# Performance work log

Measured on AMD Instinct MI355X. Metric: run time of the kernel, lower is better.

## Reference

```python
import jax, jax.numpy as jnp
import numpy as np

B, H, W = 8, 64, 64
DIM1, DIM2 = 384, 256
NH, DH = 8, 32
INNER = NH * DH
EPS = 1e-5


def _layernorm(x, w, b):
    mu = jnp.mean(x, axis=-1, keepdims=True)
    var = jnp.mean((x - mu) ** 2, axis=-1, keepdims=True)
    return (x - mu) * jax.lax.rsqrt(var + EPS) * w + b


def _axial_attn(q, k, v, scale):
    # q,k,v: [B,H,W,nh,dh]; row attention over H, col attention over W
    sh = jnp.einsum('biwnd,bjwnd->bwnij', q, k) * scale  # [B,W,nh,H,H]
    oh = jnp.einsum('bwnij,bjwnd->biwnd', jax.nn.softmax(sh, axis=-1), v)
    sw = jnp.einsum('bhind,bhjnd->bhnij', q, k) * scale  # [B,H,nh,W,W]
    ow = jnp.einsum('bhnij,bhjnd->bhind', jax.nn.softmax(sw, axis=-1), v)
    return oh + ow  # [B,H,W,nh,dh]


def setup_inputs() -> dict:
    key = jax.random.key(0)
    ks = jax.random.split(key, 16)
    s1 = 1.0 / np.sqrt(DIM1)
    s2 = 1.0 / np.sqrt(DIM2)
    si = 1.0 / np.sqrt(INNER)
    return {
        'x1': jax.random.normal(ks[0], (B, DIM1, H, W), jnp.float32),
        'x2': jax.random.normal(ks[1], (B, DIM2, H, W), jnp.float32),
        'ln1q_w': jnp.ones((DIM1,), jnp.float32),
        'ln1q_b': jnp.zeros((DIM1,), jnp.float32),
        'ln2kv_w': jnp.ones((DIM2,), jnp.float32),
        'ln2kv_b': jnp.zeros((DIM2,), jnp.float32),
        'Wq1': jax.random.normal(ks[2], (DIM1, INNER), jnp.float32) * s1,
        'Wkv2': jax.random.normal(ks[3], (DIM2, 2 * INNER), jnp.float32) * s2,
        'Wout1': jax.random.normal(ks[4], (INNER, DIM2), jnp.float32) * si,
        'bout1': jnp.zeros((DIM2,), jnp.float32),
        'ln2q_w': jnp.ones((DIM2,), jnp.float32),
        'ln2q_b': jnp.zeros((DIM2,), jnp.float32),
        'ln1kv_w': jnp.ones((DIM1,), jnp.float32),
        'ln1kv_b': jnp.zeros((DIM1,), jnp.float32),
        'Wq2': jax.random.normal(ks[5], (DIM2, INNER), jnp.float32) * s2,
        'Wkv1': jax.random.normal(ks[6], (DIM1, 2 * INNER), jnp.float32) * s1,
        'Wout2': jax.random.normal(ks[7], (INNER, DIM2), jnp.float32) * si,
        'bout2': jnp.zeros((DIM2,), jnp.float32),
        'Wsc': jax.random.normal(ks[8], (DIM2, DIM1), jnp.float32) * s1,  # 1x1 conv [out,in]
        'bn_gamma': jnp.ones((DIM2,), jnp.float32),
        'bn_beta': jnp.zeros((DIM2,), jnp.float32),
        'bn_mean': jnp.zeros((DIM2,), jnp.float32),
        'bn_var': jnp.ones((DIM2,), jnp.float32),
    }


def reference(x1, x2, ln1q_w, ln1q_b, ln2kv_w, ln2kv_b, Wq1, Wkv2, Wout1, bout1,
              ln2q_w, ln2q_b, ln1kv_w, ln1kv_b, Wq2, Wkv1, Wout2, bout2,
              Wsc, bn_gamma, bn_beta, bn_mean, bn_var):
    b, c1, h, w = x1.shape
    scale = DH ** -0.5
    x1f = jnp.transpose(x1, (0, 2, 3, 1))  # [B,H,W,C1]
    x2f = jnp.transpose(x2, (0, 2, 3, 1))  # [B,H,W,C2]

    def heads(t):
        return t.reshape(b, h, w, NH, DH)

    # branch 1: q from x1, kv from x2
    q1 = _layernorm(x1f, ln1q_w, ln1q_b) @ Wq1
    kv2 = _layernorm(x2f, ln2kv_w, ln2kv_b) @ Wkv2
    k2, v2 = jnp.split(kv2, 2, axis=-1)
    o1 = _axial_attn(heads(q1), heads(k2), heads(v2), scale)
    fused1 = o1.reshape(b, h, w, INNER) @ Wout1 + bout1
    # shortcut: 1x1 conv + BN (inference stats)
    sc = jnp.einsum('bhwc,oc->bhwo', x1f, Wsc)
    sc = (sc - bn_mean) * jax.lax.rsqrt(bn_var + EPS) * bn_gamma + bn_beta
    y1 = sc + fused1

    # branch 2: q from x2, kv from x1
    q2 = _layernorm(x2f, ln2q_w, ln2q_b) @ Wq2
    kv1 = _layernorm(x1f, ln1kv_w, ln1kv_b) @ Wkv1
    k1, v1 = jnp.split(kv1, 2, axis=-1)
    o2 = _axial_attn(heads(q2), heads(k1), heads(v1), scale)
    fused2 = o2.reshape(b, h, w, INNER) @ Wout2 + bout2
    y2 = x2f + fused2

    out = y1 + y2  # [B,H,W,C2]
    return jnp.transpose(out, (0, 3, 1, 2))
```

## Files before the change

### kernel.cpp

```cpp
#include <hip/hip_runtime.h>

typedef unsigned short u16;
typedef unsigned int u32;
typedef float v4f __attribute__((ext_vector_type(4)));
typedef __bf16 v8bf __attribute__((ext_vector_type(8)));

__device__ __forceinline__ float bf2f(u16 v) {
  union { u32 u; float f; } x; x.u = ((u32)v) << 16; return x.f;
}
__device__ __forceinline__ u16 f2bf(float f) {
  union { float f; u32 u; } x; x.f = f;
  u32 u = x.u;
  return (u16)((u + 0x7FFFu + ((u >> 16) & 1u)) >> 16);
}
__device__ __forceinline__ u32 f2u(float f) {
  union { float f; u32 u; } x; x.f = f; return x.u;
}
__device__ __forceinline__ u32 pk2bf(float a, float b) {
  const u32 au = f2u(a) + 0x8000u;
  const u32 bu = f2u(b) + 0x8000u;
  return (bu & 0xFFFF0000u) | (au >> 16);
}

struct Ptrs { const void* p[23]; };

__global__ __launch_bounds__(256) void convert_all(Ptrs ps, u16* __restrict__ cx1,
                                                   u16* __restrict__ cx2,
                                                   u16* __restrict__ cw) {
  static const int sz[23]  = {12582912, 8388608, 384, 384, 256, 256, 98304, 131072,
                              65536, 256, 256, 256, 384, 384, 65536, 196608, 65536,
                              256, 98304, 256, 256, 256, 256};
  static const int off[23] = {0, 0, 0, 384, 768, 1024, 1280, 99584, 230656, 296192,
                              296448, 296704, 296960, 297344, 297728, 363264, 559872,
                              625408, 625664, 723968, 724224, 724480, 724736};
  const int ti = blockIdx.y;
  const int n8 = sz[ti] >> 3;
  const bool isf32 = (((const u32*)ps.p[2])[0] == 0x3F800000u);
  u16* dst = (ti == 0) ? cx1 : (ti == 1) ? cx2 : (cw + off[ti]);
  const void* src = ps.p[ti];
  const int stride = gridDim.x * blockDim.x;
  for (int i = blockIdx.x * blockDim.x + threadIdx.x; i < n8; i += stride) {
    if (isf32) {
      const float4 f0 = ((const float4*)src)[2*i];
      const float4 f1 = ((const float4*)src)[2*i + 1];
      u16 tmp[8];
      tmp[0] = f2bf(f0.x); tmp[1] = f2bf(f0.y); tmp[2] = f2bf(f0.z); tmp[3] = f2bf(f0.w);
      tmp[4] = f2bf(f1.x); tmp[5] = f2bf(f1.y); tmp[6] = f2bf(f1.z); tmp[7] = f2bf(f1.w);
      ((uint4*)dst)[i] = *(const uint4*)tmp;
    } else {
      ((uint4*)dst)[i] = ((const uint4*)src)[i];
    }
  }
}

__global__ void prep_bt(const u16* __restrict__ lnq_w, const u16* __restrict__ lnq_b,
                        const u16* __restrict__ lnkv_w, const u16* __restrict__ lnkv_b,
                        const u16* __restrict__ Wq, const u16* __restrict__ Wkv,
                        u16* __restrict__ BT, float* __restrict__ bias) {
  const int C = blockDim.x;
  const int j = blockIdx.x;
  const int c = threadIdx.x;
  float w, bco, wv;
  if (j < 256) { w = bf2f(lnq_w[c]); bco = bf2f(lnq_b[c]); wv = bf2f(Wq[c*256 + j]); }
  else         { w = bf2f(lnkv_w[c]); bco = bf2f(lnkv_b[c]); wv = bf2f(Wkv[c*512 + (j-256)]); }
  BT[(size_t)j*C + c] = f2bf(w * wv);
  __shared__ float red[384];
  red[c] = bco * wv;
  __syncthreads();
  if (c == 0) { float s = 0.f; for (int i = 0; i < C; i++) s += red[i]; bias[j] = s; }
}

__global__ void prep_fin(const u16* __restrict__ Wout1, const u16* __restrict__ Wout2,
                         const u16* __restrict__ Wsc, const u16* __restrict__ bout1,
                         const u16* __restrict__ bout2, const u16* __restrict__ gam,
                         const u16* __restrict__ bet, const u16* __restrict__ mean,
                         const u16* __restrict__ var, u16* __restrict__ BT,
                         float* __restrict__ bias) {
  const int o = blockIdx.x, t = threadIdx.x;
  const float g = rsqrtf(bf2f(var[o]) + 1e-5f) * bf2f(gam[o]);
  for (int idx = t; idx < 1408; idx += 256) {
    float v;
    if (idx < 512)       v = bf2f(Wout1[(idx & 255)*256 + o]);
    else if (idx < 1024) v = bf2f(Wout2[((idx - 512) & 255)*256 + o]);
    else                 v = bf2f(Wsc[o*384 + (idx - 1024)]) * g;
    BT[(size_t)o*1408 + idx] = f2bf(v);
  }
  if (t == 0) bias[o] = bf2f(bet[o]) - bf2f(mean[o])*g + bf2f(bout1[o]) + bf2f(bout2[o]);
}

__global__ __launch_bounds__(256) void ln_c384(const u16* __restrict__ x,
                                               u16* __restrict__ xn, u16* __restrict__ xraw) {
  __shared__ u16 tile[384*66];
  __shared__ float rsum[4][64], rsq[4][64], smean[64], srstd[64];
  const int t = threadIdx.x, w = t & 63, g = t >> 6;
  const int bh = blockIdx.x, b = bh >> 6, h = bh & 63;
  const u16* src = x + (size_t)b*384*4096 + h*64 + w;
  float sum = 0.f, sq = 0.f;
  for (int j = 0; j < 96; j++) {
    const int c = g*96 + j;
    const u16 uv = src[(size_t)c*4096];
    tile[c*66 + w] = uv;
    const float v = bf2f(uv); sum += v; sq += v*v;
  }
  rsum[g][w] = sum; rsq[g][w] = sq;
  __syncthreads();
  if (t < 64) {
    const float s = rsum[0][t]+rsum[1][t]+rsum[2][t]+rsum[3][t];
    const float q = rsq[0][t]+rsq[1][t]+rsq[2][t]+rsq[3][t];
    const float mean = s * (1.0f/384.0f);
    float var = q * (1.0f/384.0f) - mean*mean;
    if (var < 0.f) var = 0.f;
    smean[t] = mean; srstd[t] = rsqrtf(var + 1e-5f);
  }
  __syncthreads();
  const size_t pos0 = (size_t)bh * 64;
  for (int i = 0; i < 96; i++) {
    const int flat = i*256 + t;
    const int ww = flat / 384, c = flat - ww*384;
    const u16 uv = tile[c*66 + ww];
    const float v = (bf2f(uv) - smean[ww]) * srstd[ww];
    const size_t p = pos0 + ww;
    xn[p*384 + c] = f2bf(v);
    xraw[p*384 + c] = uv;
  }
}

__global__ __launch_bounds__(256) void ln_c256(const u16* __restrict__ x,
                                               u16* __restrict__ xn) {
  __shared__ u16 tile[256*66];
  __shared__ float rsum[4][64], rsq[4][64], smean[64], srstd[64];
  const int t = threadIdx.x, w = t & 63, g = t >> 6;
  const int bh = blockIdx.x, b = bh >> 6, h = bh & 63;
  const u16* src = x + (size_t)b*256*4096 + h*64 + w;
  float sum = 0.f, sq = 0.f;
  for (int j = 0; j < 64; j++) {
    const int c = g*64 + j;
    const u16 uv = src[(size_t)c*4096];
    tile[c*66 + w] = uv;
    const float v = bf2f(uv); sum += v; sq += v*v;
  }
  rsum[g][w] = sum; rsq[g][w] = sq;
  __syncthreads();
  if (t < 64) {
    const float s = rsum[0][t]+rsum[1][t]+rsum[2][t]+rsum[3][t];
    const float q = rsq[0][t]+rsq[1][t]+rsq[2][t]+rsq[3][t];
    const float mean = s * (1.0f/256.0f);
    float var = q * (1.0f/256.0f) - mean*mean;
    if (var < 0.f) var = 0.f;
    smean[t] = mean; srstd[t] = rsqrtf(var + 1e-5f);
  }
  __syncthreads();
  const size_t pos0 = (size_t)bh * 64;
  for (int i = 0; i < 64; i++) {
    const int flat = i*256 + t;
    const int ww = flat >> 8, c = flat & 255;
    const float v = (bf2f(tile[c*66 + ww]) - smean[ww]) * srstd[ww];
    xn[(pos0 + ww)*256 + c] = f2bf(v);
  }
}

__global__ __launch_bounds__(256) void gemm_bt(const u16* __restrict__ A,
                                               const u16* __restrict__ BT,
                                               u16* __restrict__ C,
                                               const float* __restrict__ bias,
                                               int N, int K) {
  __shared__ u16 lsA[128*40];
  __shared__ u16 lsB[128*40];
  const int t = threadIdx.x;
  const int m0 = blockIdx.x * 128, n0 = blockIdx.y * 128;
  const int lane = t & 63, wv = t >> 6;
  const int wm = wv & 1, wn = wv >> 1;
  const int lo = lane & 15, hi = lane >> 4;
  const int r0 = t >> 2, c8 = (t & 3) << 3;
  const u16* Ab = A + (size_t)(m0 + r0) * K + c8;
  const u16* Bb = BT + (size_t)(n0 + r0) * K + c8;
  v4f acc[4][4] = {};
  for (int kb = 0; kb < K; kb += 32) {
    uint4 a0 = *(const uint4*)(Ab + kb);
    uint4 a1 = *(const uint4*)(Ab + (size_t)64*K + kb);
    uint4 b0 = *(const uint4*)(Bb + kb);
    uint4 b1 = *(const uint4*)(Bb + (size_t)64*K + kb);
    __syncthreads();
    *(uint4*)&lsA[r0*40 + c8] = a0;
    *(uint4*)&lsA[(r0+64)*40 + c8] = a1;
    *(uint4*)&lsB[r0*40 + c8] = b0;
    *(uint4*)&lsB[(r0+64)*40 + c8] = b1;
    __syncthreads();
    v8bf av[4], bv[4];
#pragma unroll
    for (int i = 0; i < 4; i++) av[i] = *(const v8bf*)&lsA[(wm*64 + i*16 + lo)*40 + hi*8];
#pragma unroll
    for (int i = 0; i < 4; i++) bv[i] = *(const v8bf*)&lsB[(wn*64 + i*16 + lo)*40 + hi*8];
#pragma unroll
    for (int mt = 0; mt < 4; mt++)
#pragma unroll
      for (int nt = 0; nt < 4; nt++)
        acc[mt][nt] = __builtin_amdgcn_mfma_f32_16x16x32_bf16(av[mt], bv[nt], acc[mt][nt], 0, 0, 0);
  }
#pragma unroll
  for (int mt = 0; mt < 4; mt++) {
    const int row = m0 + wm*64 + mt*16 + hi*4;
#pragma unroll
    for (int nt = 0; nt < 4; nt++) {
      const int col = n0 + wn*64 + nt*16 + lo;
      const float bs = bias[col];
#pragma unroll
      for (int r = 0; r < 4; r++)
        C[(size_t)(row + r) * N + col] = f2bf(acc[mt][nt][r] + bs);
    }
  }
}

__global__ __launch_bounds__(256) void gemm_final(const u16* __restrict__ Ao,
                                                  const u16* __restrict__ Ar,
                                                  const u16* __restrict__ BT,
                                                  const float* __restrict__ bias,
                                                  const u16* __restrict__ x2c,
                                                  const u32* __restrict__ probe,
                                                  void* __restrict__ outv) {
  __shared__ u16 smem[16640];
  u16* lsA = smem;
  u16* lsB = smem + 5120;
  const int t = threadIdx.x;
  const int m0 = blockIdx.x * 128, n0 = blockIdx.y * 128;
  const int lane = t & 63, wv = t >> 6;
  const int wm = wv & 1, wn = wv >> 1;
  const int lo = lane & 15, hi = lane >> 4;
  const int r0 = t >> 2, c8 = (t & 3) << 3;
  const u16* AoR = Ao + (size_t)(m0 + r0) * 1024 + c8;
  const u16* ArR = Ar + (size_t)(m0 + r0) * 384 + c8;
  const u16* Bb  = BT + (size_t)(n0 + r0) * 1408 + c8;
  v4f acc[4][4] = {};
  for (int kb = 0; kb < 1408; kb += 32) {
    uint4 a0, a1;
    if (kb < 1024) { a0 = *(const uint4*)(AoR + kb); a1 = *(const uint4*)(AoR + 64*1024 + kb); }
    else { a0 = *(const uint4*)(ArR + (kb-1024)); a1 = *(const uint4*)(ArR + 64*384 + (kb-1024)); }
    uint4 b0 = *(const uint4*)(Bb + kb);
    uint4 b1 = *(const uint4*)(Bb + 64*1408 + kb);
    __syncthreads();
    *(uint4*)&lsA[r0*40 + c8] = a0;
    *(uint4*)&lsA[(r0+64)*40 + c8] = a1;
    *(uint4*)&lsB[r0*40 + c8] = b0;
    *(uint4*)&lsB[(r0+64)*40 + c8] = b1;
    __syncthreads();
    v8bf av[4], bv[4];
#pragma unroll
    for (int i = 0; i < 4; i++) av[i] = *(const v8bf*)&lsA[(wm*64 + i*16 + lo)*40 + hi*8];
#pragma unroll
    for (int i = 0; i < 4; i++) bv[i] = *(const v8bf*)&lsB[(wn*64 + i*16 + lo)*40 + hi*8];
#pragma unroll
    for (int mt = 0; mt < 4; mt++)
#pragma unroll
      for (int nt = 0; nt < 4; nt++)
        acc[mt][nt] = __builtin_amdgcn_mfma_f32_16x16x32_bf16(av[mt], bv[nt], acc[mt][nt], 0, 0, 0);
  }
  __syncthreads();
#pragma unroll
  for (int mt = 0; mt < 4; mt++)
#pragma unroll
    for (int nt = 0; nt < 4; nt++) {
      const int nl = wn*64 + nt*16 + lo;
      const float bs = bias[n0 + nl];
#pragma unroll
      for (int r = 0; r < 4; r++)
        smem[(wm*64 + mt*16 + hi*4 + r)*130 + nl] = f2bf(acc[mt][nt][r] + bs);
    }
  __syncthreads();
  const bool isf32 = (probe[0] == 0x3F800000u);
  const int bh0 = blockIdx.x * 2;
  for (int i = 0; i < 64; i++) {
    const int flat = i*256 + t;
    const int nl = flat >> 7;
    const int rem = flat & 127;
    const int mb = rem >> 6, w = rem & 63;
    const int bh = bh0 + mb, b = bh >> 6, h = bh & 63;
    const size_t oidx = ((size_t)(b*256 + n0 + nl)*64 + h)*64 + w;
    const float val = bf2f(smem[(mb*64 + w)*130 + nl]) + bf2f(x2c[oidx]);
    if (isf32) ((float*)outv)[oidx] = val;
    else       ((u16*)outv)[oidx]   = f2bf(val);
  }
}

__global__ __launch_bounds__(64) void attn(const u16* __restrict__ qkv1,
                                           const u16* __restrict__ qkv2,
                                           u16* __restrict__ Ao) {
  __shared__ u16 smem[7424];
  constexpr int LVT = 0, LQ = 2304, LK = 4864, LP = 2304, LO = 2304;
  const int t = threadIdx.x;
  const int lo = t & 15, quad = t >> 4;
  const int bx = blockIdx.x;
  const int head = blockIdx.y;
  const int z = blockIdx.z;
  const int br = z >> 1, dir = z & 1;
  const int b = bx >> 6, x = bx & 63;
  const u16* Qb  = (br == 0) ? qkv1 : qkv2;
  const u16* KVb = (br == 0) ? qkv2 : qkv1;
  const int qc = head*32, kc = 256 + head*32, vc = 512 + head*32;
  const int pbase = (dir == 0) ? (b*4096 + x) : ((b*64 + x)*64);
  const int pstr  = (dir == 0) ? 64 : 1;
  {
    const size_t p = (size_t)(pbase + t*pstr) * 768;
    const u16* qr = Qb + p + qc;
    const u16* kr = KVb + p + kc;
    const u16* vr = KVb + p + vc;
#pragma unroll
    for (int i = 0; i < 4; i++) *(uint4*)&smem[LQ + t*40 + i*8] = *(const uint4*)(qr + i*8);
#pragma unroll
    for (int i = 0; i < 4; i++) *(uint4*)&smem[LK + t*40 + i*8] = *(const uint4*)(kr + i*8);
    u16 vbuf[32];
#pragma unroll
    for (int i = 0; i < 4; i++) *(uint4*)&vbuf[i*8] = *(const uint4*)(vr + i*8);
#pragma unroll
    for (int d = 0; d < 32; d++) smem[LVT + d*72 + t] = vbuf[d];
  }
  __syncthreads();
  v4f s[4][4];
  {
    v8bf qa[4], ka[4];
#pragma unroll
    for (int i = 0; i < 4; i++) qa[i] = *(const v8bf*)&smem[LQ + (i*16 + lo)*40 + quad*8];
#pragma unroll
    for (int i = 0; i < 4; i++) ka[i] = *(const v8bf*)&smem[LK + (i*16 + lo)*40 + quad*8];
#pragma unroll
    for (int qt = 0; qt < 4; qt++)
#pragma unroll
      for (int kt = 0; kt < 4; kt++) {
        v4f z4 = {};
        s[qt][kt] = __builtin_amdgcn_mfma_f32_16x16x32_bf16(ka[kt], qa[qt], z4, 0, 0, 0);
      }
  }
  __syncthreads();
  const float scale = 0.17677669529663687f;
#pragma unroll
  for (int qt = 0; qt < 4; qt++) {
    float tv[16];
    float mx = -1e30f;
#pragma unroll
    for (int kt = 0; kt < 4; kt++)
#pragma unroll
      for (int r = 0; r < 4; r++) {
        const float v = s[qt][kt][r] * scale;
        tv[kt*4 + r] = v;
        mx = fmaxf(mx, v);
      }
    mx = fmaxf(mx, __shfl_xor(mx, 16));
    mx = fmaxf(mx, __shfl_xor(mx, 32));
    float sm = 0.f;
#pragma unroll
    for (int i = 0; i < 16; i++) { tv[i] = __expf(tv[i] - mx); sm += tv[i]; }
    sm += __shfl_xor(sm, 16);
    sm += __shfl_xor(sm, 32);
    const float inv = 1.0f / sm;
    const int q = qt*16 + lo;
#pragma unroll
    for (int kt = 0; kt < 4; kt++)
#pragma unroll
      for (int rp = 0; rp < 2; rp++) {
        const u32 pk = pk2bf(tv[kt*4 + rp*2] * inv, tv[kt*4 + rp*2 + 1] * inv);
        *(u32*)&smem[LP + q*72 + kt*16 + quad*4 + rp*2] = pk;
      }
  }
  __syncthreads();
  v4f o[2][4] = {};
  {
    v8bf va[2][2], pb[4][2];
#pragma unroll
    for (int mt = 0; mt < 2; mt++)
#pragma unroll
      for (int ks = 0; ks < 2; ks++)
        va[mt][ks] = *(const v8bf*)&smem[LVT + (mt*16 + lo)*72 + ks*32 + quad*8];
#pragma unroll
    for (int nt = 0; nt < 4; nt++)
#pragma unroll
      for (int ks = 0; ks < 2; ks++)
        pb[nt][ks] = *(const v8bf*)&smem[LP + (nt*16 + lo)*72 + ks*32 + quad*8];
#pragma unroll
    for (int mt = 0; mt < 2; mt++)
#pragma unroll
      for (int nt = 0; nt < 4; nt++) {
        o[mt][nt] = __builtin_amdgcn_mfma_f32_16x16x32_bf16(va[mt][0], pb[nt][0], o[mt][nt], 0, 0, 0);
        o[mt][nt] = __builtin_amdgcn_mfma_f32_16x16x32_bf16(va[mt][1], pb[nt][1], o[mt][nt], 0, 0, 0);
      }
  }
  __syncthreads();
#pragma unroll
  for (int mt = 0; mt < 2; mt++)
#pragma unroll
    for (int nt = 0; nt < 4; nt++)
#pragma unroll
      for (int rp = 0; rp < 2; rp++) {
        const u32 pk = pk2bf(o[mt][nt][rp*2], o[mt][nt][rp*2 + 1]);
        *(u32*)&smem[LO + (nt*16 + lo)*40 + mt*16 + quad*4 + rp*2] = pk;
      }
  __syncthreads();
  {
    const int oc = z*256 + head*32;
    const size_t gbase = (size_t)(pbase + t*pstr) * 1024 + oc;
#pragma unroll
    for (int i = 0; i < 4; i++)
      *(uint4*)&Ao[gbase + i*8] = *(const uint4*)&smem[LO + t*40 + i*8];
  }
}

extern "C" void kernel_launch(void* const* d_in, const int* in_sizes, int n_in,
                              void* d_out, int out_size, void* d_ws, size_t ws_size,
                              hipStream_t stream) {
  char* ws = (char*)d_ws;
  u16* Ao    = (u16*)(ws);
  u16* Araw  = (u16*)(ws + 67108864);
  u16* qkv1  = (u16*)(ws + 92274688);
  u16* qkv2  = (u16*)(ws + 142606336);
  u16* cx2   = (u16*)(ws + 192937984);
  u16* cw    = (u16*)(ws + 209715200);
  u16* BT1   = (u16*)(ws + 211165184);
  u16* BT2   = (u16*)(ws + 211755008);
  u16* BTf   = (u16*)(ws + 212148224);
  float* bias1 = (float*)(ws + 212869120);
  float* bias2 = (float*)(ws + 212872192);
  float* biasf = (float*)(ws + 212875264);
  u16* cx1 = qkv1;
  u16* x1n = Ao;
  u16* x2n = Ao + 12582912;

  u16* c_ln1q_w = cw + 0,     *c_ln1q_b = cw + 384;
  u16* c_ln2kv_w = cw + 768,  *c_ln2kv_b = cw + 1024;
  u16* c_Wq1 = cw + 1280,     *c_Wkv2 = cw + 99584;
  u16* c_Wout1 = cw + 230656, *c_bout1 = cw + 296192;
  u16* c_ln2q_w = cw + 296448,*c_ln2q_b = cw + 296704;
  u16* c_ln1kv_w = cw + 296960,*c_ln1kv_b = cw + 297344;
  u16* c_Wq2 = cw + 297728,   *c_Wkv1 = cw + 363264;
  u16* c_Wout2 = cw + 559872, *c_bout2 = cw + 625408;
  u16* c_Wsc = cw + 625664;
  u16* c_bn_g = cw + 723968,  *c_bn_b = cw + 724224;
  u16* c_bn_m = cw + 724480,  *c_bn_v = cw + 724736;

  Ptrs ps;
  for (int i = 0; i < 23; i++) ps.p[i] = d_in[i];

  convert_all<<<dim3(512, 23), 256, 0, stream>>>(ps, cx1, cx2, cw);
  prep_bt<<<768, 384, 0, stream>>>(c_ln1q_w, c_ln1q_b, c_ln1kv_w, c_ln1kv_b, c_Wq1, c_Wkv1, BT1, bias1);
  prep_bt<<<768, 256, 0, stream>>>(c_ln2q_w, c_ln2q_b, c_ln2kv_w, c_ln2kv_b, c_Wq2, c_Wkv2, BT2, bias2);
  prep_fin<<<256, 256, 0, stream>>>(c_Wout1, c_Wout2, c_Wsc, c_bout1, c_bout2,
                                    c_bn_g, c_bn_b, c_bn_m, c_bn_v, BTf, biasf);
  ln_c384<<<512, 256, 0, stream>>>(cx1, x1n, Araw);
  ln_c256<<<512, 256, 0, stream>>>(cx2, x2n);
  gemm_bt<<<dim3(256, 6), 256, 0, stream>>>(x1n, BT1, qkv1, bias1, 768, 384);
  gemm_bt<<<dim3(256, 6), 256, 0, stream>>>(x2n, BT2, qkv2, bias2, 768, 256);
  attn<<<dim3(512, 8, 4), 64, 0, stream>>>(qkv1, qkv2, Ao);
  gemm_final<<<dim3(256, 2), 256, 0, stream>>>(Ao, Araw, BTf, biasf, cx2,
                                               (const u32*)d_in[2], d_out);
}
```

Baseline: 378.8 us.

## Restructure axial attention: 8 heads per block, register P, head-blocked output layout

The attention kernel now handles all 8 heads in one 512-thread block, each wave owning one head. Q and K fragments are loaded straight from global memory into registers, and V is stored transposed in an XOR-swizzled LDS layout. The softmax probabilities are rearranged across lanes with shuffles into the MFMA operand layout, so they never pass through LDS and the P·V product runs per query tile. The attention output is written in a head-blocked [z*8+head][pos][32] layout, and gemm_final's A-load addressing is changed to match. The aim is fewer LDS round-trips, fewer barriers and more coalesced stores, at the cost of more shuffle work and block-wide syncs that tie the 8 waves together.

```diff
diff --git a/kernel.cpp b/kernel.cpp
--- a/kernel.cpp
+++ b/kernel.cpp
@@ -227,14 +227,19 @@
   const int wm = wv & 1, wn = wv >> 1;
   const int lo = lane & 15, hi = lane >> 4;
   const int r0 = t >> 2, c8 = (t & 3) << 3;
-  const u16* AoR = Ao + (size_t)(m0 + r0) * 1024 + c8;
   const u16* ArR = Ar + (size_t)(m0 + r0) * 384 + c8;
   const u16* Bb  = BT + (size_t)(n0 + r0) * 1408 + c8;
   v4f acc[4][4] = {};
   for (int kb = 0; kb < 1408; kb += 32) {
     uint4 a0, a1;
-    if (kb < 1024) { a0 = *(const uint4*)(AoR + kb); a1 = *(const uint4*)(AoR + 64*1024 + kb); }
-    else { a0 = *(const uint4*)(ArR + (kb-1024)); a1 = *(const uint4*)(ArR + 64*384 + (kb-1024)); }
+    if (kb < 1024) {
+      const u16* ap = Ao + ((size_t)(kb >> 5) * 32768 + m0 + r0) * 32 + c8;
+      a0 = *(const uint4*)ap;
+      a1 = *(const uint4*)(ap + 64*32);
+    } else {
+      a0 = *(const uint4*)(ArR + (kb-1024));
+      a1 = *(const uint4*)(ArR + 64*384 + (kb-1024));
+    }
     uint4 b0 = *(const uint4*)(Bb + kb);
     uint4 b1 = *(const uint4*)(Bb + 64*1408 + kb);
     __syncthreads();
@@ -281,16 +286,16 @@
   }
 }
 
-__global__ __launch_bounds__(64) void attn(const u16* __restrict__ qkv1,
-                                           const u16* __restrict__ qkv2,
-                                           u16* __restrict__ Ao) {
-  __shared__ u16 smem[7424];
-  constexpr int LVT = 0, LQ = 2304, LK = 4864, LP = 2304, LO = 2304;
+__global__ __launch_bounds__(512) void attn(const u16* __restrict__ qkv1,
+                                            const u16* __restrict__ qkv2,
+                                            u16* __restrict__ Ao) {
+  __shared__ __attribute__((aligned(16))) u16 smem[8 * 2560];
   const int t = threadIdx.x;
-  const int lo = t & 15, quad = t >> 4;
+  const int head = t >> 6, lane = t & 63;
+  const int lo = lane & 15, quad = lane >> 4;
+  u16* sw = smem + head * 2560;
   const int bx = blockIdx.x;
-  const int head = blockIdx.y;
-  const int z = blockIdx.z;
+  const int z = blockIdx.y;
   const int br = z >> 1, dir = z & 1;
   const int b = bx >> 6, x = bx & 63;
   const u16* Qb  = (br == 0) ? qkv1 : qkv2;
@@ -298,39 +303,47 @@
   const int qc = head*32, kc = 256 + head*32, vc = 512 + head*32;
   const int pbase = (dir == 0) ? (b*4096 + x) : ((b*64 + x)*64);
   const int pstr  = (dir == 0) ? 64 : 1;
+
   {
-    const size_t p = (size_t)(pbase + t*pstr) * 768;
-    const u16* qr = Qb + p + qc;
-    const u16* kr = KVb + p + kc;
-    const u16* vr = KVb + p + vc;
-#pragma unroll
-    for (int i = 0; i < 4; i++) *(uint4*)&smem[LQ + t*40 + i*8] = *(const uint4*)(qr + i*8);
-#pragma unroll
-    for (int i = 0; i < 4; i++) *(uint4*)&smem[LK + t*40 + i*8] = *(const uint4*)(kr + i*8);
+    const u16* vr = KVb + (size_t)(pbase + lane*pstr)*768 + vc;
     u16 vbuf[32];
 #pragma unroll
     for (int i = 0; i < 4; i++) *(uint4*)&vbuf[i*8] = *(const uint4*)(vr + i*8);
-#pragma unroll
-    for (int d = 0; d < 32; d++) smem[LVT + d*72 + t] = vbuf[d];
-  }
-  __syncthreads();
+    const int khi = lane >> 3, klo = lane & 7;
+#pragma unroll
+    for (int d = 0; d < 32; d++)
+      sw[d*64 + ((khi ^ (d & 7)) << 3) + klo] = vbuf[d];
+  }
+  __syncthreads();
+
+  v8bf qa[4], ka[4];
+#pragma unroll
+  for (int i = 0; i < 4; i++) {
+    const size_t p = (size_t)(pbase + (i*16 + lo)*pstr) * 768;
+    qa[i] = *(const v8bf*)(Qb + p + qc + quad*8);
+    ka[i] = *(const v8bf*)(KVb + p + kc + quad*8);
+  }
+
   v4f s[4][4];
-  {
-    v8bf qa[4], ka[4];
-#pragma unroll
-    for (int i = 0; i < 4; i++) qa[i] = *(const v8bf*)&smem[LQ + (i*16 + lo)*40 + quad*8];
-#pragma unroll
-    for (int i = 0; i < 4; i++) ka[i] = *(const v8bf*)&smem[LK + (i*16 + lo)*40 + quad*8];
-#pragma unroll
-    for (int qt = 0; qt < 4; qt++)
-#pragma unroll
-      for (int kt = 0; kt < 4; kt++) {
-        v4f z4 = {};
-        s[qt][kt] = __builtin_amdgcn_mfma_f32_16x16x32_bf16(ka[kt], qa[qt], z4, 0, 0, 0);
-      }
-  }
-  __syncthreads();
+#pragma unroll
+  for (int qt = 0; qt < 4; qt++)
+#pragma unroll
+    for (int kt = 0; kt < 4; kt++) {
+      v4f z4 = {};
+      s[qt][kt] = __builtin_amdgcn_mfma_f32_16x16x32_bf16(ka[kt], qa[qt], z4, 0, 0, 0);
+    }
+
+  v8bf va[2][2];
+#pragma unroll
+  for (int mt = 0; mt < 2; mt++)
+#pragma unroll
+    for (int ks = 0; ks < 2; ks++) {
+      const int d = mt*16 + lo;
+      va[mt][ks] = *(const v8bf*)&sw[d*64 + (((ks*4 + quad) ^ (d & 7)) << 3)];
+    }
+
   const float scale = 0.17677669529663687f;
+  v4f o[2][4] = {};
 #pragma unroll
   for (int qt = 0; qt < 4; qt++) {
     float tv[16];
@@ -351,54 +364,57 @@
     sm += __shfl_xor(sm, 16);
     sm += __shfl_xor(sm, 32);
     const float inv = 1.0f / sm;
-    const int q = qt*16 + lo;
+    u32 pk[4][2];
 #pragma unroll
     for (int kt = 0; kt < 4; kt++)
 #pragma unroll
+      for (int rp = 0; rp < 2; rp++)
+        pk[kt][rp] = pk2bf(tv[kt*4 + rp*2] * inv, tv[kt*4 + rp*2 + 1] * inv);
+    u32 pw[2][4];
+#pragma unroll
+    for (int ks = 0; ks < 2; ks++)
+#pragma unroll
       for (int rp = 0; rp < 2; rp++) {
-        const u32 pk = pk2bf(tv[kt*4 + rp*2] * inv, tv[kt*4 + rp*2 + 1] * inv);
-        *(u32*)&smem[LP + q*72 + kt*16 + quad*4 + rp*2] = pk;
+        const u32 v16 = (quad < 2)  ? pk[2*ks][rp]   : pk[2*ks+1][rp];
+        const u32 v32 = (quad < 2)  ? pk[2*ks+1][rp] : pk[2*ks][rp];
+        const u32 v48 = (quad & 1)  ? pk[2*ks+1][rp] : pk[2*ks][rp];
+        const u32 r16 = (u32)__shfl_xor((int)v16, 16);
+        const u32 r32 = (u32)__shfl_xor((int)v32, 32);
+        const u32 r48 = (u32)__shfl_xor((int)v48, 48);
+        const u32 wlo = (quad == 0) ? pk[2*ks][rp] : (quad == 1) ? r48 : (quad == 2) ? r32 : r16;
+        const u32 whi = (quad == 0) ? r16 : (quad == 1) ? r32 : (quad == 2) ? r48 : pk[2*ks+1][rp];
+        pw[ks][rp] = wlo;
+        pw[ks][2 + rp] = whi;
       }
-  }
-  __syncthreads();
-  v4f o[2][4] = {};
+#pragma unroll
+    for (int ks = 0; ks < 2; ks++) {
+      union { u32 u[4]; v8bf v; } pb;
+      pb.u[0] = pw[ks][0]; pb.u[1] = pw[ks][1]; pb.u[2] = pw[ks][2]; pb.u[3] = pw[ks][3];
+#pragma unroll
+      for (int mt = 0; mt < 2; mt++)
+        o[mt][qt] = __builtin_amdgcn_mfma_f32_16x16x32_bf16(va[mt][ks], pb.v, o[mt][qt], 0, 0, 0);
+    }
+  }
+
+  __syncthreads();
+#pragma unroll
+  for (int mt = 0; mt < 2; mt++)
+#pragma unroll
+    for (int nt = 0; nt < 4; nt++)
+#pragma unroll
+      for (int rp = 0; rp < 2; rp++) {
+        const u32 pkv = pk2bf(o[mt][nt][rp*2], o[mt][nt][rp*2 + 1]);
+        *(u32*)&sw[(nt*16 + lo)*40 + mt*16 + quad*4 + rp*2] = pkv;
+      }
+  __syncthreads();
   {
-    v8bf va[2][2], pb[4][2];
-#pragma unroll
-    for (int mt = 0; mt < 2; mt++)
-#pragma unroll
-      for (int ks = 0; ks < 2; ks++)
-        va[mt][ks] = *(const v8bf*)&smem[LVT + (mt*16 + lo)*72 + ks*32 + quad*8];
-#pragma unroll
-    for (int nt = 0; nt < 4; nt++)
-#pragma unroll
-      for (int ks = 0; ks < 2; ks++)
-        pb[nt][ks] = *(const v8bf*)&smem[LP + (nt*16 + lo)*72 + ks*32 + quad*8];
-#pragma unroll
-    for (int mt = 0; mt < 2; mt++)
-#pragma unroll
-      for (int nt = 0; nt < 4; nt++) {
-        o[mt][nt] = __builtin_amdgcn_mfma_f32_16x16x32_bf16(va[mt][0], pb[nt][0], o[mt][nt], 0, 0, 0);
-        o[mt][nt] = __builtin_amdgcn_mfma_f32_16x16x32_bf16(va[mt][1], pb[nt][1], o[mt][nt], 0, 0, 0);
-      }
-  }
-  __syncthreads();
-#pragma unroll
-  for (int mt = 0; mt < 2; mt++)
-#pragma unroll
-    for (int nt = 0; nt < 4; nt++)
-#pragma unroll
-      for (int rp = 0; rp < 2; rp++) {
-        const u32 pk = pk2bf(o[mt][nt][rp*2], o[mt][nt][rp*2 + 1]);
-        *(u32*)&smem[LO + (nt*16 + lo)*40 + mt*16 + quad*4 + rp*2] = pk;
-      }
-  __syncthreads();
-  {
-    const int oc = z*256 + head*32;
-    const size_t gbase = (size_t)(pbase + t*pstr) * 1024 + oc;
-#pragma unroll
-    for (int i = 0; i < 4; i++)
-      *(uint4*)&Ao[gbase + i*8] = *(const uint4*)&smem[LO + t*40 + i*8];
+    const size_t sbase = (size_t)(z*8 + head) * 32768 + pbase;
+#pragma unroll
+    for (int it = 0; it < 4; it++) {
+      const int chunk = it*64 + lane;
+      const int row = chunk >> 2, ic = chunk & 3;
+      *(uint4*)&Ao[(sbase + (size_t)row*pstr)*32 + ic*8] = *(const uint4*)&sw[row*40 + ic*8];
+    }
   }
 }
 
@@ -446,7 +462,7 @@
   ln_c256<<<512, 256, 0, stream>>>(cx2, x2n);
   gemm_bt<<<dim3(256, 6), 256, 0, stream>>>(x1n, BT1, qkv1, bias1, 768, 384);
   gemm_bt<<<dim3(256, 6), 256, 0, stream>>>(x2n, BT2, qkv2, bias2, 768, 256);
-  attn<<<dim3(512, 8, 4), 64, 0, stream>>>(qkv1, qkv2, Ao);
+  attn<<<dim3(512, 4), 512, 0, stream>>>(qkv1, qkv2, Ao);
   gemm_final<<<dim3(256, 2), 256, 0, stream>>>(Ao, Araw, BTf, biasf, cx2,
                                                (const u32*)d_in[2], d_out);
 }
```

Measured after the change: 371.1 us. 1.02x faster.
